# Kernel optimization log

Hardware: AMD Instinct MI355X
Metric: run time of the kernel (lower is better)

Reference implementation:

```python
import jax, jax.numpy as jnp
import numpy as np

N_NODES = 50000
N_EDGES = 600000
HIDDEN = 128
N_LAYERS = 5


def setup_inputs() -> dict:
    key = jax.random.key(0)
    ks = jax.random.split(key, 4)
    x = jax.random.normal(ks[0], (N_NODES, HIDDEN), dtype=jnp.float32)
    edge_index = jax.random.randint(ks[1], (2, N_EDGES), 0, N_NODES, dtype=jnp.int64)
    scale = 1.0 / np.sqrt(HIDDEN)
    Wl = jax.random.normal(ks[2], (N_LAYERS, HIDDEN, HIDDEN), dtype=jnp.float32) * scale
    Wr = jax.random.normal(ks[3], (N_LAYERS, HIDDEN, HIDDEN), dtype=jnp.float32) * scale
    b = jnp.zeros((N_LAYERS, HIDDEN), dtype=jnp.float32)
    return {"x": x, "edge_index": edge_index, "Wl": Wl, "Wr": Wr, "b": b}


def _sage_conv(x, src, dst, deg_inv, Wl, Wr, b):
    # mean aggregation of source-node features at destination nodes
    msg = x[src]                                          # [E, d] gather
    agg = jax.ops.segment_sum(msg, dst, num_segments=N_NODES)  # [N, d]
    mean = agg * deg_inv                                  # [N, d]
    # PyG SAGEConv: lin_l(aggregated) + lin_r(root), bias on lin_l
    return mean @ Wl.T + b + x @ Wr.T


def reference(x, edge_index, Wl, Wr, b):
    src, dst = edge_index[0], edge_index[1]
    deg = jax.ops.segment_sum(jnp.ones((N_EDGES,), x.dtype), dst, num_segments=N_NODES)
    deg_inv = (1.0 / jnp.maximum(deg, 1.0))[:, None]      # avoid div-by-zero for isolated nodes
    h = x
    for l in range(N_LAYERS):
        h = _sage_conv(h, src, dst, deg_inv, Wl[l], Wr[l], b[l])
        if l < N_LAYERS - 1:
            h = jax.nn.relu(h)
    return h
```

## Files before the change

### kernel.cpp

```cpp
#include <hip/hip_runtime.h>

#define N_NODES 50000
#define N_EDGES 600000
#define HID 128
#define N_LAYERS 5
#define SCAN_BLK 256
#define N_SCAN_BLOCKS ((N_NODES + SCAN_BLK - 1) / SCAN_BLK)
#define NH ((size_t)N_NODES * HID)
#define NSLICE 8
#define SL_STRIDE ((size_t)N_NODES * 16)

typedef unsigned int u32;
typedef _Float16 half8 __attribute__((ext_vector_type(8)));
typedef _Float16 half4 __attribute__((ext_vector_type(4)));
typedef _Float16 h2 __attribute__((ext_vector_type(2)));
typedef float f32x4 __attribute__((ext_vector_type(4)));
typedef u32 u32x8 __attribute__((ext_vector_type(8)));

union PK { u32 u; _Float16 h[2]; };

__device__ inline u32 pack_split(float v) {
    PK r;
    r.h[0] = (_Float16)v;
    r.h[1] = (_Float16)(v - (float)r.h[0]);
    return r.u;
}
__device__ inline float unpack_sum(u32 p) {
    PK r; r.u = p;
    return (float)r.h[0] + (float)r.h[1];
}
__device__ inline float dot2acc(u32 p, float acc) {
    h2 a = __builtin_bit_cast(h2, p);
    h2 ones; ones[0] = (_Float16)1.0f; ones[1] = (_Float16)1.0f;
    return __builtin_amdgcn_fdot2(a, ones, acc, false);
}


__global__ void zero_deg(int* __restrict__ deg) {
    int i = blockIdx.x * blockDim.x + threadIdx.x;
    if (i < N_NODES) deg[i] = 0;
}

__global__ void deg_count(const int* __restrict__ dst, int* __restrict__ deg) {
    int e = blockIdx.x * blockDim.x + threadIdx.x;
    if (e < N_EDGES) atomicAdd(&deg[dst[e]], 1);
}

__global__ __launch_bounds__(SCAN_BLK) void deg_reduce(const int* __restrict__ deg,
                                                       int* __restrict__ block_sums) {
    __shared__ int s[SCAN_BLK];
    int i = blockIdx.x * SCAN_BLK + threadIdx.x;
    int v = (i < N_NODES) ? deg[i] : 0;
    s[threadIdx.x] = v;
    __syncthreads();
    for (int off = SCAN_BLK / 2; off > 0; off >>= 1) {
        if (threadIdx.x < off) s[threadIdx.x] += s[threadIdx.x + off];
        __syncthreads();
    }
    if (threadIdx.x == 0) block_sums[blockIdx.x] = s[0];
}

__global__ __launch_bounds__(SCAN_BLK) void scan_partials(const int* __restrict__ block_sums,
                                                          int* __restrict__ block_off) {
    __shared__ int s[SCAN_BLK];
    int t = threadIdx.x;
    int v = (t < N_SCAN_BLOCKS) ? block_sums[t] : 0;
    s[t] = v;
    __syncthreads();
    for (int off = 1; off < SCAN_BLK; off <<= 1) {
        int u = (t >= off) ? s[t - off] : 0;
        __syncthreads();
        s[t] += u;
        __syncthreads();
    }
    if (t < N_SCAN_BLOCKS) block_off[t] = s[t] - v;
}

__global__ __launch_bounds__(SCAN_BLK) void scan_write(const int* __restrict__ deg,
        const int* __restrict__ block_off, int* __restrict__ row_ptr,
        int* __restrict__ cursor, float* __restrict__ deg_inv) {
    __shared__ int s[SCAN_BLK];
    int t = threadIdx.x;
    int i = blockIdx.x * SCAN_BLK + t;
    int v = (i < N_NODES) ? deg[i] : 0;
    s[t] = v;
    __syncthreads();
    for (int off = 1; off < SCAN_BLK; off <<= 1) {
        int u = (t >= off) ? s[t - off] : 0;
        __syncthreads();
        s[t] += u;
        __syncthreads();
    }
    int excl = s[t] - v + block_off[blockIdx.x];
    if (i < N_NODES) {
        row_ptr[i] = excl;
        cursor[i]  = excl;
        deg_inv[i] = 1.0f / (float)max(v, 1);
    }
    if (i == N_NODES) row_ptr[N_NODES] = excl;
}

__global__ void fill_csr(const int* __restrict__ src, const int* __restrict__ dst,
                         int* __restrict__ cursor, int* __restrict__ col) {
    int e = blockIdx.x * blockDim.x + threadIdx.x;
    if (e < N_EDGES) {
        int d = dst[e];
        int pos = atomicAdd(&cursor[d], 1);
        col[pos] = src[e];
    }
}


__global__ void split_sep(const float* __restrict__ src,
                          _Float16* __restrict__ hi, _Float16* __restrict__ lo, int n4) {
    int i = blockIdx.x * blockDim.x + threadIdx.x;
    if (i >= n4) return;
    float4 v = *(const float4*)(src + (size_t)i * 4);
    half4 h, l;
    h.x = (_Float16)v.x; l.x = (_Float16)(v.x - (float)h.x);
    h.y = (_Float16)v.y; l.y = (_Float16)(v.y - (float)h.y);
    h.z = (_Float16)v.z; l.z = (_Float16)(v.z - (float)h.z);
    h.w = (_Float16)v.w; l.w = (_Float16)(v.w - (float)h.w);
    *(half4*)(hi + (size_t)i * 4) = h;
    *(half4*)(lo + (size_t)i * 4) = l;
}

__global__ void split_pk_sl(const float* __restrict__ src, u32* __restrict__ dst, int nq) {
    int i = blockIdx.x * blockDim.x + threadIdx.x;
    if (i >= nq) return;
    int n = i >> 5;
    int c = i & 31;
    float4 v = *(const float4*)(src + (size_t)n * HID + c * 4);
    uint4 r;
    r.x = pack_split(v.x); r.y = pack_split(v.y);
    r.z = pack_split(v.z); r.w = pack_split(v.w);
    int slice = c >> 2, rem = (c & 3) * 4;
    *(uint4*)(dst + (size_t)slice * SL_STRIDE + (size_t)n * 16 + rem) = r;
}


__global__ __launch_bounds__(256) void aggregate_d2(const u32* __restrict__ hp,
        const int* __restrict__ row_ptr, const int* __restrict__ col,
        const float* __restrict__ deg_inv, u32* __restrict__ mp) {
    const int wave  = threadIdx.x >> 6;
    const int lane  = threadIdx.x & 63;
    const int grp   = lane >> 2;
    const int q4    = (lane & 3) * 4;
    const int slice = blockIdx.x & 7;
    const int node  = (blockIdx.x >> 3) * 64 + wave * 16 + grp;
    if (node >= N_NODES) return;
    const u32* hsl = hp + (size_t)slice * SL_STRIDE + q4;
    const int beg = row_ptr[node], end = row_ptr[node + 1];
    float a0 = 0.f, a1 = 0.f, a2 = 0.f, a3 = 0.f;
    int e = beg;
    for (; e + 3 < end; e += 4) {
        int s0 = col[e], s1 = col[e + 1], s2 = col[e + 2], s3 = col[e + 3];
        uint4 v0 = *(const uint4*)(hsl + (unsigned)s0 * 16u);
        uint4 v1 = *(const uint4*)(hsl + (unsigned)s1 * 16u);
        uint4 v2 = *(const uint4*)(hsl + (unsigned)s2 * 16u);
        uint4 v3 = *(const uint4*)(hsl + (unsigned)s3 * 16u);
        a0 = dot2acc(v0.x, a0); a1 = dot2acc(v0.y, a1);
        a2 = dot2acc(v0.z, a2); a3 = dot2acc(v0.w, a3);
        a0 = dot2acc(v1.x, a0); a1 = dot2acc(v1.y, a1);
        a2 = dot2acc(v1.z, a2); a3 = dot2acc(v1.w, a3);
        a0 = dot2acc(v2.x, a0); a1 = dot2acc(v2.y, a1);
        a2 = dot2acc(v2.z, a2); a3 = dot2acc(v2.w, a3);
        a0 = dot2acc(v3.x, a0); a1 = dot2acc(v3.y, a1);
        a2 = dot2acc(v3.z, a2); a3 = dot2acc(v3.w, a3);
    }
    for (; e < end; ++e) {
        uint4 v0 = *(const uint4*)(hsl + (unsigned)col[e] * 16u);
        a0 = dot2acc(v0.x, a0); a1 = dot2acc(v0.y, a1);
        a2 = dot2acc(v0.z, a2); a3 = dot2acc(v0.w, a3);
    }
    const float di = deg_inv[node];
    uint4 r;
    r.x = pack_split(a0 * di);
    r.y = pack_split(a1 * di);
    r.z = pack_split(a2 * di);
    r.w = pack_split(a3 * di);
    *(uint4*)(mp + (size_t)slice * SL_STRIDE + (size_t)node * 16 + q4) = r;
}


__device__ inline void unpk8(u32x8 p, half8& hi, half8& lo) {
    #pragma unroll
    for (int i = 0; i < 8; ++i) {
        PK t; t.u = p[i];
        hi[i] = t.h[0];
        lo[i] = t.h[1];
    }
}

__global__ __launch_bounds__(512, 3) void gemm_mfma(
        const u32* __restrict__ mean_pk, const u32* __restrict__ h_pk,
        const _Float16* __restrict__ Wlh, const _Float16* __restrict__ Wll,
        const _Float16* __restrict__ Wrh, const _Float16* __restrict__ Wrl,
        const float* __restrict__ bias,
        u32* __restrict__ out_pk, float* __restrict__ out_f32, int final_layer) {
    __shared__ char Wlds[65536];
    const int t    = threadIdx.x;
    const int lane = t & 63;
    const int w    = t >> 6;
    const int jr   = lane & 15;
    const int q    = lane >> 4;

    const int basew = blockIdx.x * 128 + w * 16;
    int r0 = basew + jr; if (r0 > N_NODES - 1) r0 = N_NODES - 1;

    f32x4 accL[8], accR[8];
    #pragma unroll
    for (int jt = 0; jt < 8; ++jt) { accL[jt] = (f32x4)(0.f); accR[jt] = (f32x4)(0.f); }

    #pragma unroll
    for (int i = 0; i < 4; ++i) {
        int gi = t + i * 512;
        int j = gi >> 4, p = gi & 15;
        int dstb = j * 256 + ((p ^ (j & 7)) * 16);
        int srci = j * HID + p * 8;
        *(half8*)&Wlds[dstb]         = *(const half8*)(Wlh + srci);
        *(half8*)&Wlds[32768 + dstb] = *(const half8*)(Wrh + srci);
    }
    __syncthreads();

    half8 mhs[4], hhs[4];
    #pragma unroll
    for (int kk = 0; kk < 4; ++kk) {
        size_t a = ((size_t)(2 * kk + (q >> 1)) * N_NODES + r0) * 16 + (q & 1) * 8;
        u32x8 mp8 = *(const u32x8*)(mean_pk + a);
        u32x8 hp8 = *(const u32x8*)(h_pk + a);
        half8 mh, ml, hh, hl;
        unpk8(mp8, mh, ml); unpk8(hp8, hh, hl);
        mhs[kk] = mh; hhs[kk] = hh;
        #pragma unroll
        for (int jt = 0; jt < 8; ++jt) {
            int j  = jt * 16 + jr;
            int wb = j * 256 + (((kk * 4 + q) ^ (j & 7)) * 16);
            half8 wl = *(const half8*)&Wlds[wb];
            half8 wr = *(const half8*)&Wlds[32768 + wb];
            accL[jt] = __builtin_amdgcn_mfma_f32_16x16x32_f16(mh, wl, accL[jt], 0, 0, 0);
            accL[jt] = __builtin_amdgcn_mfma_f32_16x16x32_f16(ml, wl, accL[jt], 0, 0, 0);
            accR[jt] = __builtin_amdgcn_mfma_f32_16x16x32_f16(hh, wr, accR[jt], 0, 0, 0);
            accR[jt] = __builtin_amdgcn_mfma_f32_16x16x32_f16(hl, wr, accR[jt], 0, 0, 0);
        }
    }
    __syncthreads();

    #pragma unroll
    for (int i = 0; i < 4; ++i) {
        int gi = t + i * 512;
        int j = gi >> 4, p = gi & 15;
        int dstb = j * 256 + ((p ^ (j & 7)) * 16);
        int srci = j * HID + p * 8;
        *(half8*)&Wlds[dstb]         = *(const half8*)(Wll + srci);
        *(half8*)&Wlds[32768 + dstb] = *(const half8*)(Wrl + srci);
    }
    __syncthreads();
    #pragma unroll
    for (int kk = 0; kk < 4; ++kk) {
        half8 mh = mhs[kk], hh = hhs[kk];
        #pragma unroll
        for (int jt = 0; jt < 8; ++jt) {
            int j  = jt * 16 + jr;
            int wb = j * 256 + (((kk * 4 + q) ^ (j & 7)) * 16);
            half8 wl = *(const half8*)&Wlds[wb];
            half8 wr = *(const half8*)&Wlds[32768 + wb];
            accL[jt] = __builtin_amdgcn_mfma_f32_16x16x32_f16(mh, wl, accL[jt], 0, 0, 0);
            accR[jt] = __builtin_amdgcn_mfma_f32_16x16x32_f16(hh, wr, accR[jt], 0, 0, 0);
        }
    }

    float bv[8];
    #pragma unroll
    for (int jt = 0; jt < 8; ++jt) bv[jt] = bias[jt * 16 + jr];

    #pragma unroll
    for (int jt = 0; jt < 8; ++jt) {
        #pragma unroll
        for (int g = 0; g < 4; ++g) {
            int row = basew + q * 4 + g;
            if (row < N_NODES) {
                float v = accL[jt][g] + accR[jt][g] + bv[jt];
                if (final_layer) {
                    out_f32[(size_t)row * HID + jt * 16 + jr] = v;
                } else {
                    out_pk[((size_t)jt * N_NODES + row) * 16 + jr] =
                        pack_split(fmaxf(v, 0.f));
                }
            }
        }
    }
}


extern "C" void kernel_launch(void* const* d_in, const int* in_sizes, int n_in,
                              void* d_out, int out_size, void* d_ws, size_t ws_size,
                              hipStream_t stream) {
    const float* x    = (const float*)d_in[0];
    const int*   edge = (const int*)d_in[1];
    const float* Wl   = (const float*)d_in[2];
    const float* Wr   = (const float*)d_in[3];
    const float* bias = (const float*)d_in[4];
    float* out = (float*)d_out;

    u32* h_pk    = (u32*)d_ws;
    u32* mean_pk = h_pk + NH;
    _Float16* Wlh = (_Float16*)(mean_pk + NH);
    _Float16* Wll = Wlh + 81920;
    _Float16* Wrh = Wll + 81920;
    _Float16* Wrl = Wrh + 81920;
    float* deg_inv = (float*)(Wrl + 81920);
    int*   deg     = (int*)(deg_inv + N_NODES);
    int*   row_ptr = deg + N_NODES;
    int*   cursor  = row_ptr + (N_NODES + 1);
    int*   colarr  = cursor + N_NODES;
    int*   blk_sums = colarr + N_EDGES;
    int*   blk_off  = blk_sums + N_SCAN_BLOCKS;

    const int* src = edge;
    const int* dst = edge + N_EDGES;

    zero_deg<<<N_SCAN_BLOCKS, SCAN_BLK, 0, stream>>>(deg);
    deg_count<<<(N_EDGES + 255) / 256, 256, 0, stream>>>(dst, deg);
    deg_reduce<<<N_SCAN_BLOCKS, SCAN_BLK, 0, stream>>>(deg, blk_sums);
    scan_partials<<<1, SCAN_BLK, 0, stream>>>(blk_sums, blk_off);
    scan_write<<<N_SCAN_BLOCKS, SCAN_BLK, 0, stream>>>(deg, blk_off, row_ptr,
                                                       cursor, deg_inv);
    fill_csr<<<(N_EDGES + 255) / 256, 256, 0, stream>>>(src, dst, cursor, colarr);

    split_sep<<<(20480 + 255) / 256, 256, 0, stream>>>(Wl, Wlh, Wll, 20480);
    split_sep<<<(20480 + 255) / 256, 256, 0, stream>>>(Wr, Wrh, Wrl, 20480);
    split_pk_sl<<<(1600000 + 255) / 256, 256, 0, stream>>>(x, h_pk, 1600000);

    const int agg_blocks = ((N_NODES + 63) / 64) * NSLICE;
    const int gemm_blocks = (N_NODES + 127) / 128;

    for (int l = 0; l < N_LAYERS; ++l) {
        aggregate_d2<<<agg_blocks, 256, 0, stream>>>(
            h_pk, row_ptr, colarr, deg_inv, mean_pk);
        gemm_mfma<<<gemm_blocks, 512, 0, stream>>>(
            mean_pk, h_pk,
            Wlh + (size_t)l * 16384, Wll + (size_t)l * 16384,
            Wrh + (size_t)l * 16384, Wrl + (size_t)l * 16384,
            bias + (size_t)l * HID,
            h_pk, out, (l == N_LAYERS - 1) ? 1 : 0);
    }
}
```

Measured before the change: 404.0 us.

## Merge split kernels, unroll aggregation by 8, give each GEMM wave 32 rows

Fuses the three weight/feature split kernels into one launch. Adds an 8-way unrolled edge loop in the aggregation so more gathers are in flight per thread. Restructures the MFMA GEMM to 256-thread blocks where each wave handles 32 rows (two 16-row tiles), so each LDS weight fragment is reused twice. The trade-off is roughly double the accumulator registers per wave and fewer waves per block, which may lower occupancy.

```diff
diff --git a/kernel.cpp b/kernel.cpp
--- a/kernel.cpp
+++ b/kernel.cpp
@@ -25,10 +25,6 @@
     r.h[1] = (_Float16)(v - (float)r.h[0]);
     return r.u;
 }
-__device__ inline float unpack_sum(u32 p) {
-    PK r; r.u = p;
-    return (float)r.h[0] + (float)r.h[1];
-}
 __device__ inline float dot2acc(u32 p, float acc) {
     h2 a = __builtin_bit_cast(h2, p);
     h2 ones; ones[0] = (_Float16)1.0f; ones[1] = (_Float16)1.0f;
@@ -110,32 +106,40 @@
     }
 }
 
-
-__global__ void split_sep(const float* __restrict__ src,
-                          _Float16* __restrict__ hi, _Float16* __restrict__ lo, int n4) {
+#define W_N4 20480
+#define X_Q 1600000
+
+__global__ void split_all(const float* __restrict__ Wl, const float* __restrict__ Wr,
+                          const float* __restrict__ x,
+                          _Float16* __restrict__ Wlh, _Float16* __restrict__ Wll,
+                          _Float16* __restrict__ Wrh, _Float16* __restrict__ Wrl,
+                          u32* __restrict__ hp) {
     int i = blockIdx.x * blockDim.x + threadIdx.x;
-    if (i >= n4) return;
-    float4 v = *(const float4*)(src + (size_t)i * 4);
-    half4 h, l;
-    h.x = (_Float16)v.x; l.x = (_Float16)(v.x - (float)h.x);
-    h.y = (_Float16)v.y; l.y = (_Float16)(v.y - (float)h.y);
-    h.z = (_Float16)v.z; l.z = (_Float16)(v.z - (float)h.z);
-    h.w = (_Float16)v.w; l.w = (_Float16)(v.w - (float)h.w);
-    *(half4*)(hi + (size_t)i * 4) = h;
-    *(half4*)(lo + (size_t)i * 4) = l;
-}
-
-__global__ void split_pk_sl(const float* __restrict__ src, u32* __restrict__ dst, int nq) {
-    int i = blockIdx.x * blockDim.x + threadIdx.x;
-    if (i >= nq) return;
-    int n = i >> 5;
-    int c = i & 31;
-    float4 v = *(const float4*)(src + (size_t)n * HID + c * 4);
-    uint4 r;
-    r.x = pack_split(v.x); r.y = pack_split(v.y);
-    r.z = pack_split(v.z); r.w = pack_split(v.w);
-    int slice = c >> 2, rem = (c & 3) * 4;
-    *(uint4*)(dst + (size_t)slice * SL_STRIDE + (size_t)n * 16 + rem) = r;
+    if (i < 2 * W_N4) {
+        const float* srcp = (i < W_N4) ? Wl : Wr;
+        _Float16* hi = (i < W_N4) ? Wlh : Wrh;
+        _Float16* lo = (i < W_N4) ? Wll : Wrl;
+        int k = (i < W_N4) ? i : i - W_N4;
+        float4 v = *(const float4*)(srcp + (size_t)k * 4);
+        half4 h, l;
+        h.x = (_Float16)v.x; l.x = (_Float16)(v.x - (float)h.x);
+        h.y = (_Float16)v.y; l.y = (_Float16)(v.y - (float)h.y);
+        h.z = (_Float16)v.z; l.z = (_Float16)(v.z - (float)h.z);
+        h.w = (_Float16)v.w; l.w = (_Float16)(v.w - (float)h.w);
+        *(half4*)(hi + (size_t)k * 4) = h;
+        *(half4*)(lo + (size_t)k * 4) = l;
+    } else {
+        int iq = i - 2 * W_N4;
+        if (iq >= X_Q) return;
+        int n = iq >> 5;
+        int c = iq & 31;
+        float4 v = *(const float4*)(x + (size_t)n * HID + c * 4);
+        uint4 r;
+        r.x = pack_split(v.x); r.y = pack_split(v.y);
+        r.z = pack_split(v.z); r.w = pack_split(v.w);
+        int slice = c >> 2, rem = (c & 3) * 4;
+        *(uint4*)(hp + (size_t)slice * SL_STRIDE + (size_t)n * 16 + rem) = r;
+    }
 }
 
 
@@ -153,6 +157,34 @@
     const int beg = row_ptr[node], end = row_ptr[node + 1];
     float a0 = 0.f, a1 = 0.f, a2 = 0.f, a3 = 0.f;
     int e = beg;
+    for (; e + 7 < end; e += 8) {
+        int s0 = col[e],     s1 = col[e + 1], s2 = col[e + 2], s3 = col[e + 3];
+        int s4 = col[e + 4], s5 = col[e + 5], s6 = col[e + 6], s7 = col[e + 7];
+        uint4 v0 = *(const uint4*)(hsl + (unsigned)s0 * 16u);
+        uint4 v1 = *(const uint4*)(hsl + (unsigned)s1 * 16u);
+        uint4 v2 = *(const uint4*)(hsl + (unsigned)s2 * 16u);
+        uint4 v3 = *(const uint4*)(hsl + (unsigned)s3 * 16u);
+        uint4 v4 = *(const uint4*)(hsl + (unsigned)s4 * 16u);
+        uint4 v5 = *(const uint4*)(hsl + (unsigned)s5 * 16u);
+        uint4 v6 = *(const uint4*)(hsl + (unsigned)s6 * 16u);
+        uint4 v7 = *(const uint4*)(hsl + (unsigned)s7 * 16u);
+        a0 = dot2acc(v0.x, a0); a1 = dot2acc(v0.y, a1);
+        a2 = dot2acc(v0.z, a2); a3 = dot2acc(v0.w, a3);
+        a0 = dot2acc(v1.x, a0); a1 = dot2acc(v1.y, a1);
+        a2 = dot2acc(v1.z, a2); a3 = dot2acc(v1.w, a3);
+        a0 = dot2acc(v2.x, a0); a1 = dot2acc(v2.y, a1);
+        a2 = dot2acc(v2.z, a2); a3 = dot2acc(v2.w, a3);
+        a0 = dot2acc(v3.x, a0); a1 = dot2acc(v3.y, a1);
+        a2 = dot2acc(v3.z, a2); a3 = dot2acc(v3.w, a3);
+        a0 = dot2acc(v4.x, a0); a1 = dot2acc(v4.y, a1);
+        a2 = dot2acc(v4.z, a2); a3 = dot2acc(v4.w, a3);
+        a0 = dot2acc(v5.x, a0); a1 = dot2acc(v5.y, a1);
+        a2 = dot2acc(v5.z, a2); a3 = dot2acc(v5.w, a3);
+        a0 = dot2acc(v6.x, a0); a1 = dot2acc(v6.y, a1);
+        a2 = dot2acc(v6.z, a2); a3 = dot2acc(v6.w, a3);
+        a0 = dot2acc(v7.x, a0); a1 = dot2acc(v7.y, a1);
+        a2 = dot2acc(v7.z, a2); a3 = dot2acc(v7.w, a3);
+    }
     for (; e + 3 < end; e += 4) {
         int s0 = col[e], s1 = col[e + 1], s2 = col[e + 2], s3 = col[e + 3];
         uint4 v0 = *(const uint4*)(hsl + (unsigned)s0 * 16u);
@@ -192,7 +224,7 @@
     }
 }
 
-__global__ __launch_bounds__(512, 3) void gemm_mfma(
+__global__ __launch_bounds__(256, 2) void gemm_mfma(
         const u32* __restrict__ mean_pk, const u32* __restrict__ h_pk,
         const _Float16* __restrict__ Wlh, const _Float16* __restrict__ Wll,
         const _Float16* __restrict__ Wrh, const _Float16* __restrict__ Wrl,
@@ -205,16 +237,20 @@
     const int jr   = lane & 15;
     const int q    = lane >> 4;
 
-    const int basew = blockIdx.x * 128 + w * 16;
-    int r0 = basew + jr; if (r0 > N_NODES - 1) r0 = N_NODES - 1;
-
-    f32x4 accL[8], accR[8];
-    #pragma unroll
-    for (int jt = 0; jt < 8; ++jt) { accL[jt] = (f32x4)(0.f); accR[jt] = (f32x4)(0.f); }
-
-    #pragma unroll
-    for (int i = 0; i < 4; ++i) {
-        int gi = t + i * 512;
+    const int basew = blockIdx.x * 128 + w * 32;
+    int r0 = basew + jr;      if (r0 > N_NODES - 1) r0 = N_NODES - 1;
+    int r1 = basew + 16 + jr; if (r1 > N_NODES - 1) r1 = N_NODES - 1;
+
+    f32x4 accL0[8], accR0[8], accL1[8], accR1[8];
+    #pragma unroll
+    for (int jt = 0; jt < 8; ++jt) {
+        accL0[jt] = (f32x4)(0.f); accR0[jt] = (f32x4)(0.f);
+        accL1[jt] = (f32x4)(0.f); accR1[jt] = (f32x4)(0.f);
+    }
+
+    #pragma unroll
+    for (int i = 0; i < 8; ++i) {
+        int gi = t + i * 256;
         int j = gi >> 4, p = gi & 15;
         int dstb = j * 256 + ((p ^ (j & 7)) * 16);
         int srci = j * HID + p * 8;
@@ -223,32 +259,41 @@
     }
     __syncthreads();
 
-    half8 mhs[4], hhs[4];
+    half8 mhs0[4], hhs0[4], mhs1[4], hhs1[4];
     #pragma unroll
     for (int kk = 0; kk < 4; ++kk) {
-        size_t a = ((size_t)(2 * kk + (q >> 1)) * N_NODES + r0) * 16 + (q & 1) * 8;
-        u32x8 mp8 = *(const u32x8*)(mean_pk + a);
-        u32x8 hp8 = *(const u32x8*)(h_pk + a);
-        half8 mh, ml, hh, hl;
-        unpk8(mp8, mh, ml); unpk8(hp8, hh, hl);
-        mhs[kk] = mh; hhs[kk] = hh;
+        size_t a0 = ((size_t)(2 * kk + (q >> 1)) * N_NODES + r0) * 16 + (q & 1) * 8;
+        size_t a1 = ((size_t)(2 * kk + (q >> 1)) * N_NODES + r1) * 16 + (q & 1) * 8;
+        u32x8 m0 = *(const u32x8*)(mean_pk + a0);
+        u32x8 h0 = *(const u32x8*)(h_pk + a0);
+        u32x8 m1 = *(const u32x8*)(mean_pk + a1);
+        u32x8 h1 = *(const u32x8*)(h_pk + a1);
+        half8 mh0, ml0, hh0, hl0, mh1, ml1, hh1, hl1;
+        unpk8(m0, mh0, ml0); unpk8(h0, hh0, hl0);
+        unpk8(m1, mh1, ml1); unpk8(h1, hh1, hl1);
+        mhs0[kk] = mh0; hhs0[kk] = hh0;
+        mhs1[kk] = mh1; hhs1[kk] = hh1;
         #pragma unroll
         for (int jt = 0; jt < 8; ++jt) {
             int j  = jt * 16 + jr;
             int wb = j * 256 + (((kk * 4 + q) ^ (j & 7)) * 16);
             half8 wl = *(const half8*)&Wlds[wb];
             half8 wr = *(const half8*)&Wlds[32768 + wb];
-            accL[jt] = __builtin_amdgcn_mfma_f32_16x16x32_f16(mh, wl, accL[jt], 0, 0, 0);
-            accL[jt] = __builtin_amdgcn_mfma_f32_16x16x32_f16(ml, wl, accL[jt], 0, 0, 0);
-            accR[jt] = __builtin_amdgcn_mfma_f32_16x16x32_f16(hh, wr, accR[jt], 0, 0, 0);
-            accR[jt] = __builtin_amdgcn_mfma_f32_16x16x32_f16(hl, wr, accR[jt], 0, 0, 0);
+            accL0[jt] = __builtin_amdgcn_mfma_f32_16x16x32_f16(mh0, wl, accL0[jt], 0, 0, 0);
+            accL0[jt] = __builtin_amdgcn_mfma_f32_16x16x32_f16(ml0, wl, accL0[jt], 0, 0, 0);
+            accR0[jt] = __builtin_amdgcn_mfma_f32_16x16x32_f16(hh0, wr, accR0[jt], 0, 0, 0);
+            accR0[jt] = __builtin_amdgcn_mfma_f32_16x16x32_f16(hl0, wr, accR0[jt], 0, 0, 0);
+            accL1[jt] = __builtin_amdgcn_mfma_f32_16x16x32_f16(mh1, wl, accL1[jt], 0, 0, 0);
+            accL1[jt] = __builtin_amdgcn_mfma_f32_16x16x32_f16(ml1, wl, accL1[jt], 0, 0, 0);
+            accR1[jt] = __builtin_amdgcn_mfma_f32_16x16x32_f16(hh1, wr, accR1[jt], 0, 0, 0);
+            accR1[jt] = __builtin_amdgcn_mfma_f32_16x16x32_f16(hl1, wr, accR1[jt], 0, 0, 0);
         }
     }
     __syncthreads();
 
     #pragma unroll
-    for (int i = 0; i < 4; ++i) {
-        int gi = t + i * 512;
+    for (int i = 0; i < 8; ++i) {
+        int gi = t + i * 256;
         int j = gi >> 4, p = gi & 15;
         int dstb = j * 256 + ((p ^ (j & 7)) * 16);
         int srci = j * HID + p * 8;
@@ -258,15 +303,18 @@
     __syncthreads();
     #pragma unroll
     for (int kk = 0; kk < 4; ++kk) {
-        half8 mh = mhs[kk], hh = hhs[kk];
+        half8 mh0 = mhs0[kk], hh0 = hhs0[kk];
+        half8 mh1 = mhs1[kk], hh1 = hhs1[kk];
         #pragma unroll
         for (int jt = 0; jt < 8; ++jt) {
             int j  = jt * 16 + jr;
             int wb = j * 256 + (((kk * 4 + q) ^ (j & 7)) * 16);
             half8 wl = *(const half8*)&Wlds[wb];
             half8 wr = *(const half8*)&Wlds[32768 + wb];
-            accL[jt] = __builtin_amdgcn_mfma_f32_16x16x32_f16(mh, wl, accL[jt], 0, 0, 0);
-            accR[jt] = __builtin_amdgcn_mfma_f32_16x16x32_f16(hh, wr, accR[jt], 0, 0, 0);
+            accL0[jt] = __builtin_amdgcn_mfma_f32_16x16x32_f16(mh0, wl, accL0[jt], 0, 0, 0);
+            accR0[jt] = __builtin_amdgcn_mfma_f32_16x16x32_f16(hh0, wr, accR0[jt], 0, 0, 0);
+            accL1[jt] = __builtin_amdgcn_mfma_f32_16x16x32_f16(mh1, wl, accL1[jt], 0, 0, 0);
+            accR1[jt] = __builtin_amdgcn_mfma_f32_16x16x32_f16(hh1, wr, accR1[jt], 0, 0, 0);
         }
     }
 
@@ -280,11 +328,21 @@
         for (int g = 0; g < 4; ++g) {
             int row = basew + q * 4 + g;
             if (row < N_NODES) {
-                float v = accL[jt][g] + accR[jt][g] + bv[jt];
+                float v = accL0[jt][g] + accR0[jt][g] + bv[jt];
                 if (final_layer) {
                     out_f32[(size_t)row * HID + jt * 16 + jr] = v;
                 } else {
                     out_pk[((size_t)jt * N_NODES + row) * 16 + jr] =
+                        pack_split(fmaxf(v, 0.f));
+                }
+            }
+            int row2 = basew + 16 + q * 4 + g;
+            if (row2 < N_NODES) {
+                float v = accL1[jt][g] + accR1[jt][g] + bv[jt];
+                if (final_layer) {
+                    out_f32[(size_t)row2 * HID + jt * 16 + jr] = v;
+                } else {
+                    out_pk[((size_t)jt * N_NODES + row2) * 16 + jr] =
                         pack_split(fmaxf(v, 0.f));
                 }
             }
@@ -328,9 +386,9 @@
                                                        cursor, deg_inv);
     fill_csr<<<(N_EDGES + 255) / 256, 256, 0, stream>>>(src, dst, cursor, colarr);
 
-    split_sep<<<(20480 + 255) / 256, 256, 0, stream>>>(Wl, Wlh, Wll, 20480);
-    split_sep<<<(20480 + 255) / 256, 256, 0, stream>>>(Wr, Wrh, Wrl, 20480);
-    split_pk_sl<<<(1600000 + 255) / 256, 256, 0, stream>>>(x, h_pk, 1600000);
+    const int split_units = 2 * W_N4 + X_Q;
+    split_all<<<(split_units + 255) / 256, 256, 0, stream>>>(
+        Wl, Wr, x, Wlh, Wll, Wrh, Wrl, h_pk);
 
     const int agg_blocks = ((N_NODES + 63) / 64) * NSLICE;
     const int gemm_blocks = (N_NODES + 127) / 128;
@@ -338,7 +396,7 @@
     for (int l = 0; l < N_LAYERS; ++l) {
         aggregate_d2<<<agg_blocks, 256, 0, stream>>>(
             h_pk, row_ptr, colarr, deg_inv, mean_pk);
-        gemm_mfma<<<gemm_blocks, 512, 0, stream>>>(
+        gemm_mfma<<<gemm_blocks, 256, 0, stream>>>(
             mean_pk, h_pk,
             Wlh + (size_t)l * 16384, Wll + (size_t)l * 16384,
             Wrh + (size_t)l * 16384, Wrl + (size_t)l * 16384,
```

Result: faster. 364.0 us (median of 3 runs) (-9.9%).
